# Kernel optimization log

Hardware: AMD Instinct MI355X
Metric: run time of the kernel (lower is better)

## Reference

```python
import jax, jax.numpy as jnp
import numpy as np

N_NODES = 100000
IN_DIM = 500
HID = 64
N_CLASSES = 47
N_EDGES = 1200000
K_LAYERS = 2


def _spmm_rownorm(edge_index, h, n):
    # Row-normalized D^{-1} A @ h via gather + segment_sum over edge list.
    src, dst = edge_index[0], edge_index[1]
    ones = jnp.ones(src.shape[0], dtype=h.dtype)
    deg = jax.ops.segment_sum(ones, src, num_segments=n)
    inv_deg = 1.0 / jnp.maximum(deg, 1.0)
    msg = h[dst] * inv_deg[src][:, None]  # [E, HID]
    return jax.ops.segment_sum(msg, src, num_segments=n)  # [N, HID]


def setup_inputs() -> dict:
    key = jax.random.key(0)
    ks = jax.random.split(key, 12)
    x = jax.random.normal(ks[0], (N_NODES, IN_DIM), dtype=jnp.float32)
    edge_index_1 = jax.random.randint(ks[1], (2, N_EDGES), 0, N_NODES, dtype=jnp.int32)
    edge_index_2 = jax.random.randint(ks[2], (2, N_EDGES), 0, N_NODES, dtype=jnp.int32)
    s = 0.02
    W_embed = jax.random.normal(ks[3], (IN_DIM, HID), dtype=jnp.float32) * s
    b_embed = jnp.zeros((HID,), dtype=jnp.float32)
    W0 = jax.random.normal(ks[4], (4 * HID, HID), dtype=jnp.float32) * s
    b0 = jnp.zeros((HID,), dtype=jnp.float32)
    W1 = jax.random.normal(ks[5], (4 * HID, HID), dtype=jnp.float32) * s
    b1 = jnp.zeros((HID,), dtype=jnp.float32)
    Wc = jax.random.normal(ks[6], (HID * (K_LAYERS + 1), N_CLASSES), dtype=jnp.float32) * s
    bc = jnp.zeros((N_CLASSES,), dtype=jnp.float32)
    return {"x": x, "edge_index_1": edge_index_1, "edge_index_2": edge_index_2,
            "W_embed": W_embed, "b_embed": b_embed, "W0": W0, "b0": b0,
            "W1": W1, "b1": b1, "Wc": Wc, "bc": bc}


def reference(x, edge_index_1, edge_index_2, W_embed, b_embed, W0, b0, W1, b1, Wc, bc):
    n = x.shape[0]
    r0 = jax.nn.relu(x @ W_embed + b_embed)  # dropout = identity in eval
    reps = [r0]
    r_prev = r0
    for (W, b) in ((W0, b0), (W1, b1)):
        n1 = _spmm_rownorm(edge_index_1, r_prev, n)
        n2 = _spmm_rownorm(edge_index_2, r_prev, n)
        concat = jnp.concatenate([r_prev, n1, r_prev, n2], axis=1)  # ego separation
        r_k = jax.nn.relu(concat @ W + b)
        reps.append(r_k)
        r_prev = r_k
    emb = jnp.concatenate(reps, axis=1)  # [N, HID*(K+1)]
    logits = emb @ Wc + bc
    return logits
```

## Files before the change

kernel.cpp:

```cpp
#include <hip/hip_runtime.h>

namespace {

constexpr int N  = 100000;
constexpr int KD = 500;
constexpr int E  = 1200000;
constexpr int NC = 47;

constexpr int M2  = 2 * N;
constexpr int E2  = 2 * E;
constexpr int NB  = 391;
constexpr int AB  = 586;
constexpr int PREPB = 128;
constexpr int EBMAX = 8192;
constexpr int LDE = 128;

typedef __attribute__((ext_vector_type(8))) short short8;
typedef __attribute__((ext_vector_type(4))) float f32x4;

__device__ __forceinline__ ushort f2bf(float f) {
    union { float f; uint u; } c; c.f = f;
    uint u = c.u + 0x7fffu + ((c.u >> 16) & 1);
    return (ushort)(u >> 16);
}
__device__ __forceinline__ float bflo(uint v) { union { uint u; float f; } c; c.u = v << 16;        return c.f; }
__device__ __forceinline__ float bfhi(uint v) { union { uint u; float f; } c; c.u = v & 0xffff0000u; return c.f; }


__global__ __launch_bounds__(256) void prep_scatter(
        const float* __restrict__ We, const float* __restrict__ W0,
        const float* __restrict__ W1, const float* __restrict__ Wc,
        const float* __restrict__ bc,
        const int* __restrict__ src1, const int* __restrict__ dst1,
        const int* __restrict__ src2, const int* __restrict__ dst2,
        int* __restrict__ cursor, uint* __restrict__ ebuf,
        ushort* __restrict__ wtE, ushort* __restrict__ wf0, ushort* __restrict__ wf1,
        ushort* __restrict__ wct, float* __restrict__ bcp) {
    __shared__ int h[NB];
    __shared__ int claim[NB];
    const int t = threadIdx.x;
    if (blockIdx.x < PREPB) {
        int i = blockIdx.x * 256 + t;
        if (i < 64 * 512) {
            int c = i >> 9, k = i & 511;
            wtE[i] = f2bf(k < KD ? We[k * 64 + c] : 0.f);
        }
        if (i < 64 * 192) {
            int c = i / 192, k = i % 192;
            float v0, v1;
            if (k < 64)       { v0 = W0[k * 64 + c] + W0[(128 + k) * 64 + c];
                                v1 = W1[k * 64 + c] + W1[(128 + k) * 64 + c]; }
            else if (k < 128) { v0 = W0[k * 64 + c]; v1 = W1[k * 64 + c]; }
            else              { v0 = W0[(k + 64) * 64 + c]; v1 = W1[(k + 64) * 64 + c]; }
            wf0[i] = f2bf(v0);
            wf1[i] = f2bf(v1);
            wct[i] = f2bf(c < NC ? Wc[k * NC + c] : 0.f);
        }
        if (i < 64) bcp[i] = (i < NC) ? bc[i] : 0.f;
    } else {
        const int blk = blockIdx.x - PREPB;
        int mb[16];
        uint mu[16];
        for (int b = t; b < NB; b += 256) h[b] = 0;
        __syncthreads();
        #pragma unroll
        for (int q = 0; q < 16; ++q) {
            int i = blk * 4096 + q * 256 + t;
            if (i < E2) {
                int g = i >= E;
                int idx = i - g * E;
                int s = g ? src2[idx] : src1[idx];
                int d = g ? dst2[idx] : dst1[idx];
                int v = g * N + s;
                mb[q] = v >> 9;
                mu[q] = ((uint)(v & 511) << 17) | (uint)d;
                atomicAdd(&h[mb[q]], 1);
            } else {
                mb[q] = -1;
                mu[q] = 0;
            }
        }
        __syncthreads();
        for (int b = t; b < NB; b += 256)
            claim[b] = h[b] ? atomicAdd(&cursor[b], h[b]) : 0;
        __syncthreads();
        for (int b = t; b < NB; b += 256) h[b] = 0;
        __syncthreads();
        #pragma unroll
        for (int q = 0; q < 16; ++q) {
            if (mb[q] >= 0) {
                int r = atomicAdd(&h[mb[q]], 1);
                ebuf[(size_t)mb[q] * EBMAX + claim[mb[q]] + r] = mu[q];
            }
        }
    }
}

__global__ __launch_bounds__(256) void csr_finalize(const uint* __restrict__ ebuf, const int* __restrict__ cursor,
                                                    int* __restrict__ rp, int* __restrict__ rpe,
                                                    float* __restrict__ invd, int* __restrict__ col) {
    __shared__ uint eb[EBMAX];
    __shared__ int h[512];
    __shared__ int ex[512];
    __shared__ int ps[256];
    int bid = blockIdx.x;
    int t = threadIdx.x;
    int b0 = bid * EBMAX;
    int cnt = cursor[bid];
    if (cnt > EBMAX) cnt = EBMAX;
    if (cnt < 0) cnt = 0;
    h[t] = 0; h[t + 256] = 0;
    for (int j = t; j < cnt; j += 256) eb[j] = ebuf[b0 + j];
    __syncthreads();
    for (int j = t; j < cnt; j += 256) atomicAdd(&h[eb[j] >> 17], 1);
    __syncthreads();
    int pv = h[2 * t] + h[2 * t + 1];
    ps[t] = pv;
    __syncthreads();
    for (int off = 1; off < 256; off <<= 1) {
        int xv = (t >= off) ? ps[t - off] : 0;
        __syncthreads();
        ps[t] += xv;
        __syncthreads();
    }
    int e2 = ps[t] - pv;
    ex[2 * t] = e2;
    ex[2 * t + 1] = e2 + h[2 * t];
    __syncthreads();
    #pragma unroll
    for (int q = 0; q < 2; ++q) {
        int k = q * 256 + t;
        int n = bid * 512 + k;
        if (n < M2) {
            int st = b0 + ex[k];
            int dv = h[k];
            rp[n]  = st;
            rpe[n] = st + dv;
            invd[n] = 1.0f / (float)(dv > 1 ? dv : 1);
        }
    }
    __syncthreads();
    for (int j = t; j < cnt; j += 256) {
        uint u = eb[j];
        int ls = u >> 17;
        int r = atomicAdd(&ex[ls], 1);
        col[b0 + r] = (int)(u & 0x1FFFFu) * 256;
    }
}


__device__ __forceinline__ void stageB(const ushort* __restrict__ Wt, int ldw, int k0, short* Bs) {
    const int tid = threadIdx.x;
    #pragma unroll
    for (int i = 0; i < 2; ++i) {
        int idx = tid + i * 256;
        int c = idx >> 3, qc = (idx & 7) * 8;
        uint4 v = *reinterpret_cast<const uint4*>(Wt + (size_t)c * ldw + k0 + qc);
        *reinterpret_cast<uint4*>(Bs + (((c << 6) + qc) ^ ((c & 7) << 3))) = v;
    }
}

__device__ __forceinline__ void mma64(const short* As, const short* Bs, f32x4 acc[2][4]) {
    const int lane = threadIdx.x & 63;
    const int wrow = (threadIdx.x >> 6) * 32;
    const int llo = lane & 15, lhi = lane >> 4;
    #pragma unroll
    for (int kf = 0; kf < 2; ++kf) {
        const int kb = kf * 32 + lhi * 8;
        short8 a[2], b[4];
        #pragma unroll
        for (int m = 0; m < 2; ++m) {
            int r = wrow + m * 16 + llo;
            a[m] = *reinterpret_cast<const short8*>(As + (((r << 6) + kb) ^ ((r & 7) << 3)));
        }
        #pragma unroll
        for (int n = 0; n < 4; ++n) {
            int c = n * 16 + llo;
            b[n] = *reinterpret_cast<const short8*>(Bs + (((c << 6) + kb) ^ ((c & 7) << 3)));
        }
        #pragma unroll
        for (int m = 0; m < 2; ++m)
            #pragma unroll
            for (int n = 0; n < 4; ++n)
                acc[m][n] = __builtin_amdgcn_mfma_f32_16x16x32_bf16(a[m], b[n], acc[m][n], 0, 0, 0);
    }
}

template<bool OUTF32>
__device__ __forceinline__ void epilogue(f32x4 acc[2][4], const float* __restrict__ bias,
                                         void* out, int ldo, int ocols, int relu, int rbase) {
    const int lane = threadIdx.x & 63;
    const int wrow = (threadIdx.x >> 6) * 32;
    #pragma unroll
    for (int m = 0; m < 2; ++m) {
        #pragma unroll
        for (int r = 0; r < 4; ++r) {
            int orow = rbase + wrow + m * 16 + (lane >> 4) * 4 + r;
            if (orow >= N) continue;
            #pragma unroll
            for (int n = 0; n < 4; ++n) {
                int c = n * 16 + (lane & 15);
                float v = acc[m][n][r] + bias[c];
                if (relu) v = fmaxf(v, 0.f);
                if (OUTF32) {
                    if (c < ocols) ((float*)out)[(size_t)orow * ldo + c] = v;
                } else {
                    ((ushort*)out)[(size_t)orow * ldo + c] = f2bf(v);
                }
            }
        }
    }
}


__global__ __launch_bounds__(256) void gemm_embed(const float* __restrict__ x,
                                                  const ushort* __restrict__ WtE,
                                                  const float* __restrict__ bias,
                                                  ushort* __restrict__ out) {
    __shared__ short As[32 * 512];
    __shared__ short Bs[64 * 64];
    const int tid = threadIdx.x;
    const int rbase = blockIdx.x * 32;
    const int r = tid >> 3;
    const int j = tid & 7;
    const int swz = (r & 7) << 3;

    const float* xrow = x + (size_t)(rbase + r) * KD;
    float4 pv[16];
    #pragma unroll
    for (int i = 0; i < 16; ++i) {
        int qc = i * 32 + j * 4;
        float4 v = {0.f, 0.f, 0.f, 0.f};
        if (qc < KD) v = *reinterpret_cast<const float4*>(xrow + qc);
        pv[i] = v;
    }
    #pragma unroll
    for (int i = 0; i < 16; ++i) {
        int qc = i * 32 + j * 4;
        uint2 p;
        p.x = (uint)f2bf(pv[i].x) | ((uint)f2bf(pv[i].y) << 16);
        p.y = (uint)f2bf(pv[i].z) | ((uint)f2bf(pv[i].w) << 16);
        *reinterpret_cast<uint2*>(As + ((r << 9) + (qc ^ swz))) = p;
    }

    const int lane = tid & 63;
    const int w = tid >> 6;
    const int llo = lane & 15, lhi = lane >> 4;
    f32x4 acc[2] = {};
    for (int k0 = 0; k0 < 512; k0 += 64) {
        __syncthreads();
        stageB(WtE, 512, k0, Bs);
        __syncthreads();
        #pragma unroll
        for (int kf = 0; kf < 2; ++kf) {
            const int kbl = kf * 32 + lhi * 8;
            const int kab = k0 + kbl;
            short8 a[2], b;
            #pragma unroll
            for (int m = 0; m < 2; ++m) {
                int ar = m * 16 + llo;
                a[m] = *reinterpret_cast<const short8*>(As + ((ar << 9) + (kab ^ ((ar & 7) << 3))));
            }
            {
                int c = w * 16 + llo;
                b = *reinterpret_cast<const short8*>(Bs + (((c << 6) + kbl) ^ ((c & 7) << 3)));
            }
            #pragma unroll
            for (int m = 0; m < 2; ++m)
                acc[m] = __builtin_amdgcn_mfma_f32_16x16x32_bf16(a[m], b, acc[m], 0, 0, 0);
        }
    }

    #pragma unroll
    for (int m = 0; m < 2; ++m) {
        #pragma unroll
        for (int rr = 0; rr < 4; ++rr) {
            int orow = rbase + m * 16 + lhi * 4 + rr;
            int c = w * 16 + llo;
            float v = acc[m][rr] + bias[c];
            v = fmaxf(v, 0.f);
            out[(size_t)orow * LDE + c] = f2bf(v);
        }
    }
}


__global__ __launch_bounds__(256) void gemm3(const ushort* __restrict__ a0, int lda0,
                                             const ushort* __restrict__ a1, int lda1,
                                             const ushort* __restrict__ a2, int lda2,
                                             const ushort* __restrict__ Wt,
                                             const float* __restrict__ bias,
                                             ushort* __restrict__ out, int ldo) {
    __shared__ short As[128 * 64];
    __shared__ short Bs[64 * 64];
    const int tid = threadIdx.x;
    const int rbase = blockIdx.x * 128;
    f32x4 acc[2][4] = {};
    const ushort* aseg[3] = {a0, a1, a2};
    const int ldas[3] = {lda0, lda1, lda2};
    #pragma unroll
    for (int seg = 0; seg < 3; ++seg) {
        const ushort* A = aseg[seg];
        const int lda = ldas[seg];
        __syncthreads();
        #pragma unroll
        for (int i = 0; i < 4; ++i) {
            int idx = tid + i * 256;
            int r = idx >> 3, qc = (idx & 7) * 8;
            int grow = rbase + r;
            uint4 v = {0u, 0u, 0u, 0u};
            if (grow < N) v = *reinterpret_cast<const uint4*>(A + (size_t)grow * lda + qc);
            *reinterpret_cast<uint4*>(As + (((r << 6) + qc) ^ ((r & 7) << 3))) = v;
        }
        stageB(Wt, 192, seg * 64, Bs);
        __syncthreads();
        mma64(As, Bs, acc);
    }
    epilogue<false>(acc, bias, out, ldo, 64, 1, rbase);
}


__global__ __launch_bounds__(256) void gemm_l1cls(const ushort* __restrict__ embB,
                                                  const ushort* __restrict__ n1b,
                                                  const ushort* __restrict__ n2b,
                                                  const ushort* __restrict__ W1t,
                                                  const float* __restrict__ b1,
                                                  const ushort* __restrict__ Wct,
                                                  const float* __restrict__ bcp,
                                                  float* __restrict__ out) {
    __shared__ short As[128 * 64];
    __shared__ short Bs1[64 * 64];
    __shared__ short Bs2[64 * 64];
    const int tid = threadIdx.x;
    const int rbase = blockIdx.x * 128;
    f32x4 acc1[2][4] = {};
    f32x4 acc2[2][4] = {};

    auto stageA = [&](const ushort* A, int lda) {
        #pragma unroll
        for (int i = 0; i < 4; ++i) {
            int idx = tid + i * 256;
            int r = idx >> 3, qc = (idx & 7) * 8;
            int grow = rbase + r;
            uint4 v = {0u, 0u, 0u, 0u};
            if (grow < N) v = *reinterpret_cast<const uint4*>(A + (size_t)grow * lda + qc);
            *reinterpret_cast<uint4*>(As + (((r << 6) + qc) ^ ((r & 7) << 3))) = v;
        }
    };

    stageA(embB + 64, LDE);
    stageB(W1t, 192, 0, Bs1);
    stageB(Wct, 192, 64, Bs2);
    __syncthreads();
    mma64(As, Bs1, acc1);
    mma64(As, Bs2, acc2);
    __syncthreads();

    stageA(n1b, 64);
    stageB(W1t, 192, 64, Bs1);
    __syncthreads();
    mma64(As, Bs1, acc1);
    __syncthreads();

    stageA(n2b, 64);
    stageB(W1t, 192, 128, Bs1);
    __syncthreads();
    mma64(As, Bs1, acc1);
    __syncthreads();

    {
        const int lane = tid & 63;
        const int wrow = (tid >> 6) * 32;
        #pragma unroll
        for (int m = 0; m < 2; ++m) {
            #pragma unroll
            for (int r = 0; r < 4; ++r) {
                int row = wrow + m * 16 + (lane >> 4) * 4 + r;
                #pragma unroll
                for (int n = 0; n < 4; ++n) {
                    int c = n * 16 + (lane & 15);
                    float v = fmaxf(acc1[m][n][r] + b1[c], 0.f);
                    As[(((row << 6) + c) ^ ((row & 7) << 3))] = (short)f2bf(v);
                }
            }
        }
    }
    stageB(Wct, 192, 128, Bs1);
    __syncthreads();
    mma64(As, Bs1, acc2);
    __syncthreads();

    stageA(embB, LDE);
    stageB(Wct, 192, 0, Bs1);
    __syncthreads();
    mma64(As, Bs1, acc2);

    epilogue<true>(acc2, bcp, out, NC, NC, 0, rbase);
}


__global__ __launch_bounds__(256) void spmm7(const int* __restrict__ rp, const int* __restrict__ rpe,
                                             const int* __restrict__ col,
                                             const float* __restrict__ invd,
                                             const ushort* __restrict__ table, int colOff,
                                             ushort* __restrict__ n1b, ushort* __restrict__ n2b) {
    int gid = (blockIdx.x * 256 + threadIdx.x) >> 3;
    int ls = threadIdx.x & 7;
    if (gid >= M2) return;
    const char* hb = (const char*)(table + colOff) + ls * 16;
    float w = invd[gid];
    int s = rp[gid], e = rpe[gid];
    int e1 = e - 1;
    float a0=0.f,a1=0.f,a2=0.f,a3=0.f,a4=0.f,a5=0.f,a6=0.f,a7=0.f;
    for (int j = s; j < e; j += 8) {
        int off[8];
        float wv[8];
        #pragma unroll
        for (int u = 0; u < 8; ++u) {
            int jj = j + u;
            int cidx = jj < e ? jj : e1;
            off[u] = col[cidx];
            wv[u] = jj < e ? 1.f : 0.f;
        }
        uint4 v[8];
        #pragma unroll
        for (int u = 0; u < 8; ++u) v[u] = *reinterpret_cast<const uint4*>(hb + off[u]);
        #pragma unroll
        for (int u = 0; u < 8; ++u) {
            a0 = fmaf(wv[u], bflo(v[u].x), a0); a1 = fmaf(wv[u], bfhi(v[u].x), a1);
            a2 = fmaf(wv[u], bflo(v[u].y), a2); a3 = fmaf(wv[u], bfhi(v[u].y), a3);
            a4 = fmaf(wv[u], bflo(v[u].z), a4); a5 = fmaf(wv[u], bfhi(v[u].z), a5);
            a6 = fmaf(wv[u], bflo(v[u].w), a6); a7 = fmaf(wv[u], bfhi(v[u].w), a7);
        }
    }
    int g = gid >= N;
    int node = gid - g * N;
    ushort* op = g ? n2b : n1b;
    uint4 o;
    o.x = (uint)f2bf(a0 * w) | ((uint)f2bf(a1 * w) << 16);
    o.y = (uint)f2bf(a2 * w) | ((uint)f2bf(a3 * w) << 16);
    o.z = (uint)f2bf(a4 * w) | ((uint)f2bf(a5 * w) << 16);
    o.w = (uint)f2bf(a6 * w) | ((uint)f2bf(a7 * w) << 16);
    *reinterpret_cast<uint4*>(op + (size_t)node * 64 + ls * 8) = o;
}

}

extern "C" void kernel_launch(void* const* d_in, const int* in_sizes, int n_in,
                              void* d_out, int out_size, void* d_ws, size_t ws_size,
                              hipStream_t stream) {
    const float* x       = (const float*)d_in[0];
    const int*   ei1     = (const int*)d_in[1];
    const int*   ei2     = (const int*)d_in[2];
    const float* W_embed = (const float*)d_in[3];
    const float* b_embed = (const float*)d_in[4];
    const float* W0      = (const float*)d_in[5];
    const float* b0      = (const float*)d_in[6];
    const float* W1      = (const float*)d_in[7];
    const float* b1      = (const float*)d_in[8];
    const float* Wc      = (const float*)d_in[9];
    const float* bc      = (const float*)d_in[10];
    float* out = (float*)d_out;

    char* ws = (char*)d_ws;
    size_t off = 0;
    auto alloc = [&](size_t bytes) -> void* {
        void* p = ws + off;
        off += (bytes + 255) & ~(size_t)255;
        return p;
    };

    ushort* embB  = (ushort*)alloc((size_t)N * LDE * 2);
    ushort* n1b   = (ushort*)alloc((size_t)N * 64 * 2);
    ushort* n2b   = (ushort*)alloc((size_t)N * 64 * 2);
    int*    col   = (int*)alloc((size_t)NB * EBMAX * 4);
    uint*   ebuf  = (uint*)alloc((size_t)NB * EBMAX * 4);
    int*    rp    = (int*)alloc((size_t)M2 * 4);
    int*    rpe   = (int*)alloc((size_t)M2 * 4);
    float*  invd  = (float*)alloc((size_t)M2 * 4);
    int*    bcur  = (int*)alloc((NB + 1) * 4);
    ushort* wtE   = (ushort*)alloc(64 * 512 * 2);
    ushort* weff0 = (ushort*)alloc(64 * 192 * 2);
    ushort* weff1 = (ushort*)alloc(64 * 192 * 2);
    ushort* wct   = (ushort*)alloc(64 * 192 * 2);
    float*  bcp   = (float*)alloc(64 * 4);
    if (off > ws_size) return;

    const int* src1 = ei1, *dst1 = ei1 + E;
    const int* src2 = ei2, *dst2 = ei2 + E;

    const int GB  = (N + 127) / 128;
    const int GBE = N / 32;
    const int PB  = (M2 * 8 + 255) / 256;

    hipMemsetAsync(bcur, 0, NB * sizeof(int), stream);

    prep_scatter<<<PREPB + AB, 256, 0, stream>>>(W_embed, W0, W1, Wc, bc,
                                                 src1, dst1, src2, dst2, bcur, ebuf,
                                                 wtE, weff0, weff1, wct, bcp);

    csr_finalize<<<NB, 256, 0, stream>>>(ebuf, bcur, rp, rpe, invd, col);

    gemm_embed<<<GBE, 256, 0, stream>>>(x, wtE, b_embed, embB);

    spmm7<<<PB, 256, 0, stream>>>(rp, rpe, col, invd, embB, 0, n1b, n2b);
    gemm3<<<GB, 256, 0, stream>>>(embB, LDE, n1b, 64, n2b, 64, weff0, b0, embB + 64, LDE);

    spmm7<<<PB, 256, 0, stream>>>(rp, rpe, col, invd, embB, 64, n1b, n2b);
    gemm_l1cls<<<GB, 256, 0, stream>>>(embB, n1b, n2b, weff1, b1, wct, bcp, out);
}
```

Measured before the change: 218.5 us.

## Split gather table into two 32-column slabs for cache-friendly SpMM

The GEMM epilogues now also write their bf16 output into a column-split slab layout (two contiguous N×32 halves). The SpMM kernel is split into two passes over blocks, one per half, each gathering 64-byte rows from a 6.4 MB slab instead of 128-byte strided rows from the 25.6 MB embedding table. The aim is to keep the random-gather working set within L2 or the last-level cache. In exchange there are extra scattered 2-byte slab writes in the epilogues and twice as many SpMM threads each walking the CSR indices.

```diff
diff --git a/kernel.cpp b/kernel.cpp
--- a/kernel.cpp
+++ b/kernel.cpp
@@ -14,6 +14,7 @@
 constexpr int PREPB = 128;
 constexpr int EBMAX = 8192;
 constexpr int LDE = 128;
+constexpr int PB2 = (M2 * 4) / 256;
 
 typedef __attribute__((ext_vector_type(8))) short short8;
 typedef __attribute__((ext_vector_type(4))) float f32x4;
@@ -144,7 +145,7 @@
         uint u = eb[j];
         int ls = u >> 17;
         int r = atomicAdd(&ex[ls], 1);
-        col[b0 + r] = (int)(u & 0x1FFFFu) * 256;
+        col[b0 + r] = (int)(u & 0x1FFFFu) * 64;
     }
 }
 
@@ -188,7 +189,8 @@
 
 template<bool OUTF32>
 __device__ __forceinline__ void epilogue(f32x4 acc[2][4], const float* __restrict__ bias,
-                                         void* out, int ldo, int ocols, int relu, int rbase) {
+                                         void* out, int ldo, int ocols, int relu, int rbase,
+                                         ushort* __restrict__ slab) {
     const int lane = threadIdx.x & 63;
     const int wrow = (threadIdx.x >> 6) * 32;
     #pragma unroll
@@ -205,7 +207,9 @@
                 if (OUTF32) {
                     if (c < ocols) ((float*)out)[(size_t)orow * ldo + c] = v;
                 } else {
-                    ((ushort*)out)[(size_t)orow * ldo + c] = f2bf(v);
+                    ushort bv = f2bf(v);
+                    ((ushort*)out)[(size_t)orow * ldo + c] = bv;
+                    if (slab) slab[(size_t)(c >> 5) * (N * 32) + (size_t)orow * 32 + (c & 31)] = bv;
                 }
             }
         }
@@ -216,7 +220,8 @@
 __global__ __launch_bounds__(256) void gemm_embed(const float* __restrict__ x,
                                                   const ushort* __restrict__ WtE,
                                                   const float* __restrict__ bias,
-                                                  ushort* __restrict__ out) {
+                                                  ushort* __restrict__ out,
+                                                  ushort* __restrict__ slab) {
     __shared__ short As[32 * 512];
     __shared__ short Bs[64 * 64];
     const int tid = threadIdx.x;
@@ -279,7 +284,9 @@
             int c = w * 16 + llo;
             float v = acc[m][rr] + bias[c];
             v = fmaxf(v, 0.f);
-            out[(size_t)orow * LDE + c] = f2bf(v);
+            ushort bv = f2bf(v);
+            out[(size_t)orow * LDE + c] = bv;
+            slab[(size_t)(c >> 5) * (N * 32) + (size_t)orow * 32 + (c & 31)] = bv;
         }
     }
 }
@@ -290,7 +297,8 @@
                                              const ushort* __restrict__ a2, int lda2,
                                              const ushort* __restrict__ Wt,
                                              const float* __restrict__ bias,
-                                             ushort* __restrict__ out, int ldo) {
+                                             ushort* __restrict__ out, int ldo,
+                                             ushort* __restrict__ slab) {
     __shared__ short As[128 * 64];
     __shared__ short Bs[64 * 64];
     const int tid = threadIdx.x;
@@ -316,7 +324,7 @@
         __syncthreads();
         mma64(As, Bs, acc);
     }
-    epilogue<false>(acc, bias, out, ldo, 64, 1, rbase);
+    epilogue<false>(acc, bias, out, ldo, 64, 1, rbase, slab);
 }
 
 
@@ -395,19 +403,22 @@
     __syncthreads();
     mma64(As, Bs1, acc2);
 
-    epilogue<true>(acc2, bcp, out, NC, NC, 0, rbase);
-}
-
-
-__global__ __launch_bounds__(256) void spmm7(const int* __restrict__ rp, const int* __restrict__ rpe,
+    epilogue<true>(acc2, bcp, out, NC, NC, 0, rbase, nullptr);
+}
+
+
+__global__ __launch_bounds__(256) void spmm8(const int* __restrict__ rp, const int* __restrict__ rpe,
                                              const int* __restrict__ col,
                                              const float* __restrict__ invd,
-                                             const ushort* __restrict__ table, int colOff,
+                                             const ushort* __restrict__ slab,
                                              ushort* __restrict__ n1b, ushort* __restrict__ n2b) {
-    int gid = (blockIdx.x * 256 + threadIdx.x) >> 3;
-    int ls = threadIdx.x & 7;
+    int bid = blockIdx.x;
+    int hh = bid >= PB2;
+    int b = bid - (hh ? PB2 : 0);
+    int gid = (b * 256 + threadIdx.x) >> 2;
+    int ls = threadIdx.x & 3;
     if (gid >= M2) return;
-    const char* hb = (const char*)(table + colOff) + ls * 16;
+    const char* hb = (const char*)slab + (size_t)hh * (N * 64) + ls * 16;
     float w = invd[gid];
     int s = rp[gid], e = rpe[gid];
     int e1 = e - 1;
@@ -441,7 +452,7 @@
     o.y = (uint)f2bf(a2 * w) | ((uint)f2bf(a3 * w) << 16);
     o.z = (uint)f2bf(a4 * w) | ((uint)f2bf(a5 * w) << 16);
     o.w = (uint)f2bf(a6 * w) | ((uint)f2bf(a7 * w) << 16);
-    *reinterpret_cast<uint4*>(op + (size_t)node * 64 + ls * 8) = o;
+    *reinterpret_cast<uint4*>((char*)op + (size_t)node * 128 + hh * 64 + ls * 16) = o;
 }
 
 }
@@ -471,6 +482,7 @@
     };
 
     ushort* embB  = (ushort*)alloc((size_t)N * LDE * 2);
+    ushort* gslab = (ushort*)alloc((size_t)2 * N * 32 * 2);
     ushort* n1b   = (ushort*)alloc((size_t)N * 64 * 2);
     ushort* n2b   = (ushort*)alloc((size_t)N * 64 * 2);
     int*    col   = (int*)alloc((size_t)NB * EBMAX * 4);
@@ -491,7 +503,6 @@
 
     const int GB  = (N + 127) / 128;
     const int GBE = N / 32;
-    const int PB  = (M2 * 8 + 255) / 256;
 
     hipMemsetAsync(bcur, 0, NB * sizeof(int), stream);
 
@@ -501,11 +512,11 @@
 
     csr_finalize<<<NB, 256, 0, stream>>>(ebuf, bcur, rp, rpe, invd, col);
 
-    gemm_embed<<<GBE, 256, 0, stream>>>(x, wtE, b_embed, embB);
-
-    spmm7<<<PB, 256, 0, stream>>>(rp, rpe, col, invd, embB, 0, n1b, n2b);
-    gemm3<<<GB, 256, 0, stream>>>(embB, LDE, n1b, 64, n2b, 64, weff0, b0, embB + 64, LDE);
-
-    spmm7<<<PB, 256, 0, stream>>>(rp, rpe, col, invd, embB, 64, n1b, n2b);
+    gemm_embed<<<GBE, 256, 0, stream>>>(x, wtE, b_embed, embB, gslab);
+
+    spmm8<<<2 * PB2, 256, 0, stream>>>(rp, rpe, col, invd, gslab, n1b, n2b);
+    gemm3<<<GB, 256, 0, stream>>>(embB, LDE, n1b, 64, n2b, 64, weff0, b0, embB + 64, LDE, gslab);
+
+    spmm8<<<2 * PB2, 256, 0, stream>>>(rp, rpe, col, invd, gslab, n1b, n2b);
     gemm_l1cls<<<GB, 256, 0, stream>>>(embB, n1b, n2b, weff1, b1, wct, bcp, out);
 }
```

Result: slower. 252.9 us (+15.7%).
